# Kernel tuning notes

Hardware: AMD Instinct MI355X
Metric: run time of the kernel (lower is better)

Reference implementation:

```python
import jax, jax.numpy as jnp
import numpy as np

D_MODEL = 1024
NUM_HEADS = 16
DEPTH = D_MODEL // NUM_HEADS
EPS = 1e-6


def setup_inputs() -> dict:
    key = jax.random.key(0)
    ks = jax.random.split(key, 9)
    B, S = 4, 2048
    scale = 1.0 / np.sqrt(D_MODEL)
    inp = {
        "inputs": jax.random.normal(ks[0], (B, S, D_MODEL), dtype=jnp.float32),
        "Wq": jax.random.normal(ks[1], (D_MODEL, D_MODEL), dtype=jnp.float32) * scale,
        "bq": jnp.zeros((D_MODEL,), dtype=jnp.float32),
        "Wk": jax.random.normal(ks[2], (D_MODEL, D_MODEL), dtype=jnp.float32) * scale,
        "bk": jnp.zeros((D_MODEL,), dtype=jnp.float32),
        "Wv": jax.random.normal(ks[3], (D_MODEL, D_MODEL), dtype=jnp.float32) * scale,
        "bv": jnp.zeros((D_MODEL,), dtype=jnp.float32),
        "Wo": jax.random.normal(ks[4], (D_MODEL, D_MODEL), dtype=jnp.float32) * scale,
        "bo": jnp.zeros((D_MODEL,), dtype=jnp.float32),
        "gamma": jnp.ones((D_MODEL,), dtype=jnp.float32),
        "beta": jnp.zeros((D_MODEL,), dtype=jnp.float32),
    }
    return inp


def _layer_norm(x, gamma, beta):
    mu = jnp.mean(x, axis=-1, keepdims=True)
    var = jnp.mean(jnp.square(x - mu), axis=-1, keepdims=True)
    return (x - mu) * jax.lax.rsqrt(var + EPS) * gamma + beta


def reference(inputs, Wq, bq, Wk, bk, Wv, bv, Wo, bo, gamma, beta):
    B, S, _ = inputs.shape
    # QKV projections, split heads: [B, H, S, depth]
    def split_heads(x):
        return x.reshape(B, S, NUM_HEADS, DEPTH).transpose(0, 2, 1, 3)

    q = split_heads(inputs @ Wq + bq)
    k = split_heads(inputs @ Wk + bk)
    v = split_heads(inputs @ Wv + bv)

    # scores: [B, H, S, S]
    scores = jnp.einsum("bhqd,bhkd->bhqk", q, k) / jnp.sqrt(
        jnp.asarray(DEPTH, dtype=inputs.dtype))
    attn = jax.nn.softmax(scores, axis=-1)  # dropout is identity in eval mode
    out = jnp.einsum("bhqk,bhkd->bhqd", attn, v)
    out = out.transpose(0, 2, 1, 3).reshape(B, S, D_MODEL)
    out = out @ Wo + bo  # dropout2 identity in eval mode
    return _layer_norm(inputs + out, gamma, beta)
```

## Files before the change

kernel.cpp:

```cpp
#include <hip/hip_runtime.h>
#include <hip/hip_bf16.h>


typedef __bf16 bf16;
typedef __bf16 bf16x4 __attribute__((ext_vector_type(4)));
typedef __bf16 bf16x8 __attribute__((ext_vector_type(8)));
typedef float floatx4 __attribute__((ext_vector_type(4)));

#define MFMA16(a, b, c) __builtin_amdgcn_mfma_f32_16x16x32_bf16((a), (b), (c), 0, 0, 0)

static __device__ __forceinline__ floatx4 vmax4(floatx4 a, floatx4 b) {
    floatx4 r;
    r[0] = fmaxf(a[0], b[0]); r[1] = fmaxf(a[1], b[1]);
    r[2] = fmaxf(a[2], b[2]); r[3] = fmaxf(a[3], b[3]);
    return r;
}

__global__ __launch_bounds__(256) void convert_kernel(
    const float* __restrict__ x, bf16* __restrict__ xb)
{
    const int i = blockIdx.x * 256 + threadIdx.x;
    const float4 v = ((const float4*)x)[i];
    bf16x4 r;
    r[0] = (bf16)v.x; r[1] = (bf16)v.y; r[2] = (bf16)v.z; r[3] = (bf16)v.w;
    ((bf16x4*)xb)[i] = r;
}

__global__ __launch_bounds__(256) void transpose_kernel(
    const float* __restrict__ Wq, const float* __restrict__ Wk,
    const float* __restrict__ Wv, const float* __restrict__ Wo,
    bf16* __restrict__ WT, bf16* __restrict__ WoT)
{
    __shared__ float tile[32][33];
    const int z = blockIdx.z;
    const float* src = (z == 0) ? Wq : (z == 1) ? Wk : (z == 2) ? Wv : Wo;
    bf16* dst = (z < 3) ? (WT + (long)z * 1024 * 1024) : WoT;
    const int n0 = blockIdx.x * 32, k0 = blockIdx.y * 32;
    const int tx = threadIdx.x & 31, ty = threadIdx.x >> 5;
#pragma unroll
    for (int i = 0; i < 32; i += 8)
        tile[ty + i][tx] = src[(long)(k0 + ty + i) * 1024 + n0 + tx];
    __syncthreads();
#pragma unroll
    for (int i = 0; i < 32; i += 8)
        dst[(long)(n0 + ty + i) * 1024 + k0 + tx] = (bf16)tile[tx][ty + i];
}

template <int MODE>
__global__ __launch_bounds__(256, 2) void gemm_kernel(
    const bf16* __restrict__ A, const bf16* __restrict__ Bt,
    const float* __restrict__ b0, const float* __restrict__ b1,
    const float* __restrict__ b2, const float* __restrict__ X,
    bf16* __restrict__ Qo, bf16* __restrict__ Ko, bf16* __restrict__ Vto,
    bf16* __restrict__ Tmpb, int N, int K)
{
    constexpr int LDT = 40;
    __shared__ __align__(16) bf16 As[128 * LDT];
    __shared__ __align__(16) bf16 Bs[128 * LDT];
    const int t = threadIdx.x;
    const int lane = t & 63;
    const int w = t >> 6;
    const int wm = w >> 1, wn = w & 1;
    const int g = lane >> 4, c = lane & 15;
    const int bm = blockIdx.y * 128;
    const int bn = blockIdx.x * 128;

    const int srow = t >> 2;
    const int scol = (t & 3) * 8;

    floatx4 acc[4][4];
#pragma unroll
    for (int i = 0; i < 4; ++i)
#pragma unroll
        for (int j = 0; j < 4; ++j) acc[i][j] = floatx4{0.f, 0.f, 0.f, 0.f};

    const bf16* Ap0 = A + (long)(bm + srow) * K + scol;
    const bf16* Ap1 = A + (long)(bm + 64 + srow) * K + scol;
    const bf16* Bp0 = Bt + (long)(bn + srow) * K + scol;
    const bf16* Bp1 = Bt + (long)(bn + 64 + srow) * K + scol;

    uint4 a0 = *(const uint4*)(Ap0);
    uint4 a1 = *(const uint4*)(Ap1);
    uint4 q0 = *(const uint4*)(Bp0);
    uint4 q1 = *(const uint4*)(Bp1);

    for (int k0 = 0; k0 < K; k0 += 32) {
        __syncthreads();
        *(uint4*)&As[srow * LDT + scol] = a0;
        *(uint4*)&As[(64 + srow) * LDT + scol] = a1;
        *(uint4*)&Bs[srow * LDT + scol] = q0;
        *(uint4*)&Bs[(64 + srow) * LDT + scol] = q1;
        __syncthreads();
        if (k0 + 32 < K) {
            a0 = *(const uint4*)(Ap0 + k0 + 32);
            a1 = *(const uint4*)(Ap1 + k0 + 32);
            q0 = *(const uint4*)(Bp0 + k0 + 32);
            q1 = *(const uint4*)(Bp1 + k0 + 32);
        }
        bf16x8 af[4], bfv[4];
#pragma unroll
        for (int i = 0; i < 4; ++i)
            af[i] = *(const bf16x8*)&As[(wm * 64 + i * 16 + c) * LDT + g * 8];
#pragma unroll
        for (int j = 0; j < 4; ++j)
            bfv[j] = *(const bf16x8*)&Bs[(wn * 64 + j * 16 + c) * LDT + g * 8];
#pragma unroll
        for (int i = 0; i < 4; ++i)
#pragma unroll
            for (int j = 0; j < 4; ++j)
                acc[i][j] = MFMA16(af[i], bfv[j], acc[i][j]);
    }

    if (MODE == 0) {
#pragma unroll
        for (int j = 0; j < 4; ++j) {
            const int col = bn + wn * 64 + j * 16 + c;
            const int sec = col >> 10;
            const int nn = col & 1023;
            const int h = nn >> 6, dd = nn & 63;
            const float* bp = (sec == 0) ? b0 : (sec == 1) ? b1 : b2;
            const float bias = bp[nn];
#pragma unroll
            for (int i = 0; i < 4; ++i) {
                const int r0 = bm + wm * 64 + i * 16 + g * 4;
                if (sec == 2) {
                    bf16x4 pack;
#pragma unroll
                    for (int reg = 0; reg < 4; ++reg)
                        pack[reg] = (bf16)(acc[i][j][reg] + bias);
                    const int b_ = r0 >> 11, sr = r0 & 2047;
                    *(bf16x4*)&Vto[((long)(b_ * 16 + h) * 64 + dd) * 2048 + sr] = pack;
                } else {
#pragma unroll
                    for (int reg = 0; reg < 4; ++reg) {
                        const int r = r0 + reg;
                        const int b_ = r >> 11, sr = r & 2047;
                        const float v = acc[i][j][reg] + bias;
                        if (sec == 0)
                            Qo[((long)(b_ * 16 + h) * 2048 + sr) * 64 + dd] =
                                (bf16)(v * 0.18033688011112042f);
                        else
                            Ko[((long)(b_ * 16 + h) * 2048 + sr) * 64 + dd] = (bf16)v;
                    }
                }
            }
        }
    } else {
#pragma unroll
        for (int j = 0; j < 4; ++j) {
            const int col = bn + wn * 64 + j * 16 + c;
            const float bias = b0[col];
#pragma unroll
            for (int i = 0; i < 4; ++i) {
#pragma unroll
                for (int reg = 0; reg < 4; ++reg) {
                    const int r = bm + wm * 64 + i * 16 + g * 4 + reg;
                    Tmpb[(long)r * N + col] =
                        (bf16)(acc[i][j][reg] + bias + X[(long)r * N + col]);
                }
            }
        }
    }
}

__global__ __launch_bounds__(256, 2) void flash_kernel(
    const bf16* __restrict__ Q, const bf16* __restrict__ Kc,
    const bf16* __restrict__ Vt, bf16* __restrict__ O)
{
    constexpr int KSTR = 72;
    constexpr int VSTR = 136;
    constexpr int PSTR = 136;
    __shared__ __align__(16) bf16 Ks[128 * KSTR];
    __shared__ __align__(16) bf16 Vs[64 * VSTR];
    __shared__ __align__(16) bf16 Pl[4 * 32 * PSTR];
    const int t = threadIdx.x;
    const int lane = t & 63;
    const int w = t >> 6;
    const int g = lane >> 4, c = lane & 15;
    const int bh = blockIdx.x;
    const int b_ = bh >> 4, h = bh & 15;
    const bf16* Qp = Q + (long)bh * 2048 * 64;
    const bf16* Kp = Kc + (long)bh * 2048 * 64;
    const bf16* Vp = Vt + (long)bh * 64 * 2048;
    const int q0 = blockIdx.y * 128 + w * 32;
    bf16* Pw = Pl + w * 32 * PSTR;

    bf16x8 qf[2][2];
#pragma unroll
    for (int qs = 0; qs < 2; ++qs)
#pragma unroll
        for (int p = 0; p < 2; ++p)
            qf[qs][p] = *(const bf16x8*)(Qp + (long)(q0 + qs * 16 + c) * 64 + p * 32 + g * 8);

    float m_c[2] = {-1e30f, -1e30f};
    float l_c[2] = {0.f, 0.f};
    floatx4 o[2][4];
#pragma unroll
    for (int qs = 0; qs < 2; ++qs)
#pragma unroll
        for (int dd = 0; dd < 4; ++dd) o[qs][dd] = floatx4{0.f, 0.f, 0.f, 0.f};

    for (int kt = 0; kt < 16; ++kt) {
        __syncthreads();
        {
            uint4 kr[4], vr[4];
#pragma unroll
            for (int i = 0; i < 4; ++i) {
                const int idx = i * 256 + t;
                kr[i] = *(const uint4*)(Kp + (long)kt * 8192 + idx * 8);
                const int vd = idx >> 4, vsc = idx & 15;
                vr[i] = *(const uint4*)(Vp + (long)vd * 2048 + kt * 128 + vsc * 8);
            }
#pragma unroll
            for (int i = 0; i < 4; ++i) {
                const int idx = i * 256 + t;
                *(uint4*)&Ks[(idx >> 3) * KSTR + (idx & 7) * 8] = kr[i];
                *(uint4*)&Vs[(idx >> 4) * VSTR + (idx & 15) * 8] = vr[i];
            }
        }
        __syncthreads();

        floatx4 s[2][8];
#pragma unroll
        for (int ks = 0; ks < 8; ++ks) {
            bf16x8 kf0 = *(const bf16x8*)&Ks[(ks * 16 + c) * KSTR + g * 8];
            bf16x8 kf1 = *(const bf16x8*)&Ks[(ks * 16 + c) * KSTR + 32 + g * 8];
#pragma unroll
            for (int qs = 0; qs < 2; ++qs) {
                floatx4 z = floatx4{0.f, 0.f, 0.f, 0.f};
                z = MFMA16(kf0, qf[qs][0], z);
                z = MFMA16(kf1, qf[qs][1], z);
                s[qs][ks] = z;
            }
        }

#pragma unroll
        for (int qs = 0; qs < 2; ++qs) {
            floatx4 t0 = vmax4(s[qs][0], s[qs][1]);
            floatx4 t1 = vmax4(s[qs][2], s[qs][3]);
            floatx4 t2 = vmax4(s[qs][4], s[qs][5]);
            floatx4 t3 = vmax4(s[qs][6], s[qs][7]);
            t0 = vmax4(vmax4(t0, t1), vmax4(t2, t3));
            float mx = fmaxf(fmaxf(t0[0], t0[1]), fmaxf(t0[2], t0[3]));
            mx = fmaxf(mx, __shfl_xor(mx, 16, 64));
            mx = fmaxf(mx, __shfl_xor(mx, 32, 64));
            const float mn = fmaxf(m_c[qs], mx);
            const float al = __builtin_amdgcn_exp2f(m_c[qs] - mn);
            m_c[qs] = mn;
            floatx4 a4 = floatx4{0.f, 0.f, 0.f, 0.f};
#pragma unroll
            for (int ks = 0; ks < 8; ++ks) {
#pragma unroll
                for (int r = 0; r < 4; ++r)
                    s[qs][ks][r] = __builtin_amdgcn_exp2f(s[qs][ks][r] - mn);
                a4 += s[qs][ks];
            }
            float rs = (a4[0] + a4[1]) + (a4[2] + a4[3]);
            rs += __shfl_xor(rs, 16, 64);
            rs += __shfl_xor(rs, 32, 64);
            l_c[qs] = l_c[qs] * al + rs;
            float al_r[4];
#pragma unroll
            for (int r = 0; r < 4; ++r) al_r[r] = __shfl(al, g * 4 + r, 64);
#pragma unroll
            for (int dd = 0; dd < 4; ++dd)
#pragma unroll
                for (int r = 0; r < 4; ++r) o[qs][dd][r] *= al_r[r];
#pragma unroll
            for (int ks = 0; ks < 8; ++ks) {
                bf16x4 pk;
#pragma unroll
                for (int r = 0; r < 4; ++r) pk[r] = (bf16)s[qs][ks][r];
                *(bf16x4*)&Pw[(qs * 16 + c) * PSTR + ks * 16 + g * 4] = pk;
            }
        }
        asm volatile("s_waitcnt lgkmcnt(0)" ::: "memory");
#pragma unroll
        for (int kk = 0; kk < 4; ++kk) {
            bf16x8 pf0 = *(const bf16x8*)&Pw[(0 + c) * PSTR + kk * 32 + g * 8];
            bf16x8 pf1 = *(const bf16x8*)&Pw[(16 + c) * PSTR + kk * 32 + g * 8];
#pragma unroll
            for (int dd = 0; dd < 4; ++dd) {
                bf16x8 vf = *(const bf16x8*)&Vs[(dd * 16 + c) * VSTR + kk * 32 + g * 8];
                o[0][dd] = MFMA16(pf0, vf, o[0][dd]);
                o[1][dd] = MFMA16(pf1, vf, o[1][dd]);
            }
        }
    }

#pragma unroll
    for (int qs = 0; qs < 2; ++qs) {
        float linv[4];
#pragma unroll
        for (int r = 0; r < 4; ++r) linv[r] = 1.0f / __shfl(l_c[qs], g * 4 + r, 64);
#pragma unroll
        for (int dd = 0; dd < 4; ++dd)
#pragma unroll
            for (int r = 0; r < 4; ++r) {
                const float v = o[qs][dd][r] * linv[r];
                const int q = q0 + qs * 16 + g * 4 + r;
                O[((long)b_ * 2048 + q) * 1024 + h * 64 + dd * 16 + c] = (bf16)v;
            }
    }
}

__global__ __launch_bounds__(256, 2) void ln_kernel(
    const bf16* __restrict__ Tmp, const float* __restrict__ gamma,
    const float* __restrict__ beta, float* __restrict__ out)
{
    const int row = blockIdx.x;
    const int t = threadIdx.x;
    const int lane = t & 63, w = t >> 6;
    const bf16x4 vb = ((const bf16x4*)(Tmp + (long)row * 1024))[t];
    const float xv[4] = {(float)vb[0], (float)vb[1], (float)vb[2], (float)vb[3]};
    float s = xv[0] + xv[1] + xv[2] + xv[3];
    float ss = xv[0] * xv[0] + xv[1] * xv[1] + xv[2] * xv[2] + xv[3] * xv[3];
#pragma unroll
    for (int off = 1; off < 64; off <<= 1) {
        s += __shfl_xor(s, off, 64);
        ss += __shfl_xor(ss, off, 64);
    }
    __shared__ float sb[4], ssb[4];
    if (lane == 0) { sb[w] = s; ssb[w] = ss; }
    __syncthreads();
    s = sb[0] + sb[1] + sb[2] + sb[3];
    ss = ssb[0] + ssb[1] + ssb[2] + ssb[3];
    const float mu = s * (1.0f / 1024.0f);
    const float var = ss * (1.0f / 1024.0f) - mu * mu;
    const float inv = rsqrtf(var + 1e-6f);
    const float4 gm = ((const float4*)gamma)[t];
    const float4 bt = ((const float4*)beta)[t];
    float4 r;
    r.x = (xv[0] - mu) * inv * gm.x + bt.x;
    r.y = (xv[1] - mu) * inv * gm.y + bt.y;
    r.z = (xv[2] - mu) * inv * gm.z + bt.z;
    r.w = (xv[3] - mu) * inv * gm.w + bt.w;
    ((float4*)(out + (long)row * 1024))[t] = r;
}

extern "C" void kernel_launch(void* const* d_in, const int* in_sizes, int n_in,
                              void* d_out, int out_size, void* d_ws, size_t ws_size,
                              hipStream_t stream)
{
    const float* x     = (const float*)d_in[0];
    const float* Wq    = (const float*)d_in[1];
    const float* bq    = (const float*)d_in[2];
    const float* Wk    = (const float*)d_in[3];
    const float* bk    = (const float*)d_in[4];
    const float* Wv    = (const float*)d_in[5];
    const float* bv    = (const float*)d_in[6];
    const float* Wo    = (const float*)d_in[7];
    const float* bo    = (const float*)d_in[8];
    const float* gamma = (const float*)d_in[9];
    const float* beta  = (const float*)d_in[10];
    float* out = (float*)d_out;

    char* ws = (char*)d_ws;
    bf16* xb   = (bf16*)(ws);
    bf16* WT   = (bf16*)(ws + 16777216);
    bf16* Qb   = (bf16*)(ws + 23068672);
    bf16* Kb   = (bf16*)(ws + 39845888);
    bf16* WoT  = (bf16*)(ws + 56623104);
    bf16* Tmpb = (bf16*)(ws);
    bf16* Vtb  = (bf16*)d_out;
    bf16* Ob   = (bf16*)((char*)d_out + 16777216);

    convert_kernel<<<8192, 256, 0, stream>>>(x, xb);
    transpose_kernel<<<dim3(32, 32, 4), 256, 0, stream>>>(Wq, Wk, Wv, Wo, WT, WoT);
    gemm_kernel<0><<<dim3(24, 64), 256, 0, stream>>>(
        xb, WT, bq, bk, bv, nullptr, Qb, Kb, Vtb, nullptr, 3072, 1024);
    flash_kernel<<<dim3(64, 16), 256, 0, stream>>>(Qb, Kb, Vtb, Ob);
    gemm_kernel<1><<<dim3(8, 64), 256, 0, stream>>>(
        Ob, WoT, bo, nullptr, nullptr, x, nullptr, nullptr, nullptr, Tmpb, 1024, 1024);
    ln_kernel<<<8192, 256, 0, stream>>>(Tmpb, gamma, beta, out);
}
```

Before: 350.2 us.

## Shrink flash KV tile, prefetch next tile into registers, transpose PV output layout

```diff
diff --git a/kernel.cpp b/kernel.cpp
--- a/kernel.cpp
+++ b/kernel.cpp
@@ -163,14 +163,14 @@
     }
 }
 
-__global__ __launch_bounds__(256, 2) void flash_kernel(
+__global__ __launch_bounds__(256, 4) void flash_kernel(
     const bf16* __restrict__ Q, const bf16* __restrict__ Kc,
     const bf16* __restrict__ Vt, bf16* __restrict__ O)
 {
     constexpr int KSTR = 72;
-    constexpr int VSTR = 136;
-    constexpr int PSTR = 136;
-    __shared__ __align__(16) bf16 Ks[128 * KSTR];
+    constexpr int VSTR = 72;
+    constexpr int PSTR = 72;
+    __shared__ __align__(16) bf16 Ks[64 * KSTR];
     __shared__ __align__(16) bf16 Vs[64 * VSTR];
     __shared__ __align__(16) bf16 Pl[4 * 32 * PSTR];
     const int t = threadIdx.x;
@@ -200,29 +200,35 @@
 #pragma unroll
         for (int dd = 0; dd < 4; ++dd) o[qs][dd] = floatx4{0.f, 0.f, 0.f, 0.f};
 
-    for (int kt = 0; kt < 16; ++kt) {
+    uint4 kr[2], vr[2];
+#pragma unroll
+    for (int i = 0; i < 2; ++i) {
+        const int idx = i * 256 + t;
+        kr[i] = *(const uint4*)(Kp + (long)idx * 8);
+        vr[i] = *(const uint4*)(Vp + (long)(idx >> 3) * 2048 + (idx & 7) * 8);
+    }
+
+    for (int kt = 0; kt < 32; ++kt) {
         __syncthreads();
-        {
-            uint4 kr[4], vr[4];
-#pragma unroll
-            for (int i = 0; i < 4; ++i) {
+#pragma unroll
+        for (int i = 0; i < 2; ++i) {
+            const int idx = i * 256 + t;
+            *(uint4*)&Ks[(idx >> 3) * KSTR + (idx & 7) * 8] = kr[i];
+            *(uint4*)&Vs[(idx >> 3) * VSTR + (idx & 7) * 8] = vr[i];
+        }
+        __syncthreads();
+        if (kt + 1 < 32) {
+#pragma unroll
+            for (int i = 0; i < 2; ++i) {
                 const int idx = i * 256 + t;
-                kr[i] = *(const uint4*)(Kp + (long)kt * 8192 + idx * 8);
-                const int vd = idx >> 4, vsc = idx & 15;
-                vr[i] = *(const uint4*)(Vp + (long)vd * 2048 + kt * 128 + vsc * 8);
-            }
-#pragma unroll
-            for (int i = 0; i < 4; ++i) {
-                const int idx = i * 256 + t;
-                *(uint4*)&Ks[(idx >> 3) * KSTR + (idx & 7) * 8] = kr[i];
-                *(uint4*)&Vs[(idx >> 4) * VSTR + (idx & 15) * 8] = vr[i];
-            }
-        }
-        __syncthreads();
-
-        floatx4 s[2][8];
-#pragma unroll
-        for (int ks = 0; ks < 8; ++ks) {
+                kr[i] = *(const uint4*)(Kp + (long)(kt + 1) * 4096 + idx * 8);
+                vr[i] = *(const uint4*)(Vp + (long)(idx >> 3) * 2048 + (kt + 1) * 64 + (idx & 7) * 8);
+            }
+        }
+
+        floatx4 s[2][4];
+#pragma unroll
+        for (int ks = 0; ks < 4; ++ks) {
             bf16x8 kf0 = *(const bf16x8*)&Ks[(ks * 16 + c) * KSTR + g * 8];
             bf16x8 kf1 = *(const bf16x8*)&Ks[(ks * 16 + c) * KSTR + 32 + g * 8];
 #pragma unroll
@@ -236,11 +242,7 @@
 
 #pragma unroll
         for (int qs = 0; qs < 2; ++qs) {
-            floatx4 t0 = vmax4(s[qs][0], s[qs][1]);
-            floatx4 t1 = vmax4(s[qs][2], s[qs][3]);
-            floatx4 t2 = vmax4(s[qs][4], s[qs][5]);
-            floatx4 t3 = vmax4(s[qs][6], s[qs][7]);
-            t0 = vmax4(vmax4(t0, t1), vmax4(t2, t3));
+            floatx4 t0 = vmax4(vmax4(s[qs][0], s[qs][1]), vmax4(s[qs][2], s[qs][3]));
             float mx = fmaxf(fmaxf(t0[0], t0[1]), fmaxf(t0[2], t0[3]));
             mx = fmaxf(mx, __shfl_xor(mx, 16, 64));
             mx = fmaxf(mx, __shfl_xor(mx, 32, 64));
@@ -249,7 +251,7 @@
             m_c[qs] = mn;
             floatx4 a4 = floatx4{0.f, 0.f, 0.f, 0.f};
 #pragma unroll
-            for (int ks = 0; ks < 8; ++ks) {
+            for (int ks = 0; ks < 4; ++ks) {
 #pragma unroll
                 for (int r = 0; r < 4; ++r)
                     s[qs][ks][r] = __builtin_amdgcn_exp2f(s[qs][ks][r] - mn);
@@ -259,15 +261,12 @@
             rs += __shfl_xor(rs, 16, 64);
             rs += __shfl_xor(rs, 32, 64);
             l_c[qs] = l_c[qs] * al + rs;
-            float al_r[4];
-#pragma unroll
-            for (int r = 0; r < 4; ++r) al_r[r] = __shfl(al, g * 4 + r, 64);
 #pragma unroll
             for (int dd = 0; dd < 4; ++dd)
 #pragma unroll
-                for (int r = 0; r < 4; ++r) o[qs][dd][r] *= al_r[r];
-#pragma unroll
-            for (int ks = 0; ks < 8; ++ks) {
+                for (int r = 0; r < 4; ++r) o[qs][dd][r] *= al;
+#pragma unroll
+            for (int ks = 0; ks < 4; ++ks) {
                 bf16x4 pk;
 #pragma unroll
                 for (int r = 0; r < 4; ++r) pk[r] = (bf16)s[qs][ks][r];
@@ -276,31 +275,29 @@
         }
         asm volatile("s_waitcnt lgkmcnt(0)" ::: "memory");
 #pragma unroll
-        for (int kk = 0; kk < 4; ++kk) {
+        for (int kk = 0; kk < 2; ++kk) {
             bf16x8 pf0 = *(const bf16x8*)&Pw[(0 + c) * PSTR + kk * 32 + g * 8];
             bf16x8 pf1 = *(const bf16x8*)&Pw[(16 + c) * PSTR + kk * 32 + g * 8];
 #pragma unroll
             for (int dd = 0; dd < 4; ++dd) {
                 bf16x8 vf = *(const bf16x8*)&Vs[(dd * 16 + c) * VSTR + kk * 32 + g * 8];
-                o[0][dd] = MFMA16(pf0, vf, o[0][dd]);
-                o[1][dd] = MFMA16(pf1, vf, o[1][dd]);
+                o[0][dd] = MFMA16(vf, pf0, o[0][dd]);
+                o[1][dd] = MFMA16(vf, pf1, o[1][dd]);
             }
         }
     }
 
 #pragma unroll
     for (int qs = 0; qs < 2; ++qs) {
-        float linv[4];
-#pragma unroll
-        for (int r = 0; r < 4; ++r) linv[r] = 1.0f / __shfl(l_c[qs], g * 4 + r, 64);
-#pragma unroll
-        for (int dd = 0; dd < 4; ++dd)
-#pragma unroll
-            for (int r = 0; r < 4; ++r) {
-                const float v = o[qs][dd][r] * linv[r];
-                const int q = q0 + qs * 16 + g * 4 + r;
-                O[((long)b_ * 2048 + q) * 1024 + h * 64 + dd * 16 + c] = (bf16)v;
-            }
+        const float linv = 1.0f / l_c[qs];
+        const int q = q0 + qs * 16 + c;
+#pragma unroll
+        for (int dd = 0; dd < 4; ++dd) {
+            bf16x4 pk;
+#pragma unroll
+            for (int r = 0; r < 4; ++r) pk[r] = (bf16)(o[qs][dd][r] * linv);
+            *(bf16x4*)&O[((long)b_ * 2048 + q) * 1024 + h * 64 + dd * 16 + g * 4] = pk;
+        }
     }
 }
 
```

Measured after the change: 386.4 us. 10.3% more time.
